# Optimization experiments

Hardware: AMD Instinct MI355X
Metric: run time of the kernel (lower is better)

Reference implementation:

```python
import jax, jax.numpy as jnp
import numpy as np


def _hadamard(n: int) -> np.ndarray:
    # Sylvester construction; n must be a power of 2 (asserted in the torch source).
    H = np.array([[1.0]], dtype=np.float32)
    while H.shape[0] < n:
        H = np.block([[H, H], [H, -H]])
    return (H * (n ** -0.5)).astype(np.float32)


def _rotate_activation(x):
    # hadamard_transform(x, scale=D**-0.5) over the last dim; bf16 in/out like the CUDA kernel.
    D = x.shape[-1]
    H = jnp.asarray(_hadamard(D))
    return (x.astype(jnp.float32) @ H).astype(x.dtype)


def _cu_seqlen_kv_bounds(seq_lens, num_ctx_tokens):
    # Vectorized equivalent of compute_cu_seqlen_kv_bounds_nocache (repeat_interleave -> searchsorted).
    offsets = jnp.concatenate([jnp.zeros(1, jnp.int32), jnp.cumsum(seq_lens).astype(jnp.int32)])
    pos = jnp.arange(num_ctx_tokens, dtype=jnp.int32)
    batch_ids = jnp.searchsorted(offsets, pos, side='right').astype(jnp.int32) - 1
    ks = offsets[batch_ids]                 # start of this token's sequence in packed KV
    ke = ks + (pos - ks) + 1                # causal: local_position + 1 past the start
    return ks, ke


def setup_inputs() -> dict:
    key = jax.random.key(0)
    k1, k2, k3 = jax.random.split(key, 3)
    T, H, D = 2048, 16, 128
    q = jax.random.normal(k1, (T, H, D), dtype=jnp.bfloat16)
    k = jax.random.normal(k2, (T, D), dtype=jnp.bfloat16)
    weights = jax.random.uniform(k3, (T, H), dtype=jnp.float32) * (H ** -0.5)
    seq_lens = jnp.array([1024, 1024], dtype=jnp.int32)
    return {"q": q, "k": k, "weights": weights, "seq_lens": seq_lens, "index_topk": 256}


def reference(q, k, weights, seq_lens, index_topk):
    T = q.shape[0]
    # Hadamard-rotate q and k (lightning indexer activation rotation).
    qr = _rotate_activation(q).astype(jnp.float32)   # [T, H, D]
    kr = _rotate_activation(k).astype(jnp.float32)   # [T, D]
    # Index score: I[t, s] = sum_h w[t, h] * relu(q[t, h] . k[s])
    logits = jnp.einsum('thd,sd->ths', qr, kr)       # [T, H, T]
    scores = jnp.einsum('ths,th->ts', jax.nn.relu(logits), weights)  # [T, T]
    # Causal ragged-batch KV window per token.
    ks, ke = _cu_seqlen_kv_bounds(seq_lens, T)
    pos = jnp.arange(T, dtype=jnp.int32)
    valid = (pos[None, :] >= ks[:, None]) & (pos[None, :] < ke[:, None])
    NEG = jnp.float32(-1e30)
    masked = jnp.where(valid, scores, NEG)
    topk_vals, topk_idx = jax.lax.top_k(masked, index_topk)  # [T, topk]
    return topk_vals, topk_idx
```

## Files before the change

kernel.cpp:

```cpp
#include <hip/hip_runtime.h>
#include <hip/hip_bf16.h>
#include <stdint.h>

typedef __attribute__((ext_vector_type(8))) short short8;
typedef __attribute__((ext_vector_type(4))) float float4_t;

#define DDIM 128
#define SORTN 256
#define LROW 136
#define SCAP 1088
#define NCHT 17

__device__ inline unsigned short f32_to_bf16_rne(float f) {
    uint32_t u = __float_as_uint(f);
    return (unsigned short)((u + 0x7FFFu + ((u >> 16) & 1u)) >> 16);
}
__device__ inline float bf16_to_f32(unsigned short h) {
    return __uint_as_float(((uint32_t)h) << 16);
}
__device__ inline int ks_of(const int* seq_lens, int n_seq, int t) {
    int off = 0, r = 0;
    for (int i = 0; i < n_seq; ++i) {
        int nx = off + seq_lens[i];
        if (t < nx) { r = off; break; }
        off = nx;
    }
    return r;
}

__device__ inline int wave_reduce_add_dpp(int x) {
    x += __builtin_amdgcn_update_dpp(0, x, 0x111, 0xF, 0xF, true);
    x += __builtin_amdgcn_update_dpp(0, x, 0x112, 0xF, 0xF, true);
    x += __builtin_amdgcn_update_dpp(0, x, 0x114, 0xF, 0xF, true);
    x += __builtin_amdgcn_update_dpp(0, x, 0x118, 0xF, 0xF, true);
    x += __builtin_amdgcn_update_dpp(0, x, 0x142, 0xA, 0xF, true);
    x += __builtin_amdgcn_update_dpp(0, x, 0x143, 0xC, 0xF, true);
    return __builtin_amdgcn_readlane(x, 63);
}

__global__ __launch_bounds__(256) void rotate_k_kernel(
        const unsigned short* __restrict__ k, unsigned short* __restrict__ kr, int T) {
    int row = blockIdx.x * 16 + (threadIdx.x >> 4);
    if (row >= T) return;
    int l16 = threadIdx.x & 15;
    short8 in = *(const short8*)(k + (size_t)row * DDIM + 8 * l16);
    float f[8];
    #pragma unroll
    for (int j = 0; j < 8; ++j) f[j] = bf16_to_f32((unsigned short)in[j]);
    #pragma unroll
    for (int b = 1; b <= 4; b <<= 1)
        #pragma unroll
        for (int j = 0; j < 8; ++j)
            if (!(j & b)) { float a = f[j], c = f[j | b]; f[j] = a + c; f[j | b] = a - c; }
    #pragma unroll
    for (int m = 1; m <= 8; m <<= 1) {
        bool hi = (l16 & m) != 0;
        #pragma unroll
        for (int j = 0; j < 8; ++j) {
            float o = __shfl_xor(f[j], m, 64);
            f[j] = hi ? (o - f[j]) : (f[j] + o);
        }
    }
    const float sc = 0.08838834764831845f;
    short8 out;
    #pragma unroll
    for (int j = 0; j < 8; ++j) out[j] = (short)f32_to_bf16_rne(f[j] * sc);
    *(short8*)(kr + (size_t)row * DDIM + 8 * l16) = out;
}

__global__ __launch_bounds__(512, 4) void fused_kernel(
        const unsigned short* __restrict__ q,
        const unsigned short* __restrict__ kr,
        const float* __restrict__ w,
        const int* __restrict__ seq_lens, int n_seq,
        float* __restrict__ out_vals, float* __restrict__ out_idx,
        int T, int H, int K, int Tt) {
    __shared__ __align__(16) unsigned short bL[128 * LROW];
    __shared__ __align__(16) float scw[4][SCAP];

    const int tid  = threadIdx.x;
    const int wv   = tid >> 6, lane = tid & 63;
    const int tok  = wv & 3, half = wv >> 2;
    const int col  = lane & 15, kgrp = lane >> 4;
    const int srow = tid >> 4, sseg = tid & 15;

    const int m     = blockIdx.x;
    const int ttile = (m & 1) ? (Tt - 1 - (m >> 1)) : (m >> 1);
    const int tt0   = ttile * 4;
    const int t_w   = tt0 + tok;
    const bool wvalid = (t_w < T);
    const int t_c  = wvalid ? t_w : T - 1;
    const int ks_w = ks_of(seq_lens, n_seq, t_c);
    const int ke_w = t_c + 1;
    const int n    = ke_w - ks_w;

    const int bks   = ks_of(seq_lens, n_seq, tt0);
    const int bke   = (tt0 + 4 < T) ? (tt0 + 4) : T;
    const int ntile = (bke - bks + 127) >> 7;

    short8 pre[4];
    {
        int kv0 = bks;
        #pragma unroll
        for (int it = 0; it < 4; ++it) {
            int gs = kv0 + srow + 32 * it; if (gs > T - 1) gs = T - 1;
            pre[it] = *(const short8*)(kr + (size_t)gs * DDIM + sseg * 8);
        }
    }

    float f[4][8];
    const unsigned short* qrow = q + ((size_t)t_c * H + col) * DDIM + kgrp * 8;
    #pragma unroll
    for (int kk = 0; kk < 4; ++kk) {
        short8 v = *(const short8*)(qrow + kk * 32);
        #pragma unroll
        for (int j = 0; j < 8; ++j) f[kk][j] = bf16_to_f32((unsigned short)v[j]);
    }
    #pragma unroll
    for (int b = 1; b <= 4; b <<= 1)
        #pragma unroll
        for (int kk = 0; kk < 4; ++kk)
            #pragma unroll
            for (int j = 0; j < 8; ++j)
                if (!(j & b)) { float a = f[kk][j], c = f[kk][j | b];
                                f[kk][j] = a + c; f[kk][j | b] = a - c; }
    #pragma unroll
    for (int kk = 0; kk < 4; ++kk)
        #pragma unroll
        for (int j = 0; j < 8; ++j) {
            float o = __shfl_xor(f[kk][j], 16, 64);
            f[kk][j] = (kgrp & 1) ? (o - f[kk][j]) : (f[kk][j] + o);
        }
    #pragma unroll
    for (int kk = 0; kk < 4; ++kk)
        #pragma unroll
        for (int j = 0; j < 8; ++j) {
            float o = __shfl_xor(f[kk][j], 32, 64);
            f[kk][j] = (kgrp & 2) ? (o - f[kk][j]) : (f[kk][j] + o);
        }
    #pragma unroll
    for (int j = 0; j < 8; ++j) {
        { float a = f[0][j], c = f[1][j]; f[0][j] = a + c; f[1][j] = a - c; }
        { float a = f[2][j], c = f[3][j]; f[2][j] = a + c; f[3][j] = a - c; }
        { float a = f[0][j], c = f[2][j]; f[0][j] = a + c; f[2][j] = a - c; }
        { float a = f[1][j], c = f[3][j]; f[1][j] = a + c; f[3][j] = a - c; }
    }
    short8 afrag[4];
    const float scl = 0.08838834764831845f;
    #pragma unroll
    for (int kk = 0; kk < 4; ++kk)
        #pragma unroll
        for (int j = 0; j < 8; ++j)
            afrag[kk][j] = (short)f32_to_bf16_rne(f[kk][j] * scl);

    float w4[4];
    #pragma unroll
    for (int r = 0; r < 4; ++r) w4[r] = w[(size_t)t_c * H + kgrp * 4 + r];

    #pragma unroll
    for (int it = 0; it < 4; ++it)
        *(short8*)&bL[(srow + 32 * it) * LROW + sseg * 8] = pre[it];
    __syncthreads();

    for (int c = 0; c < ntile; ++c) {
        const int kv0 = bks + c * 128;
        if (c + 1 < ntile) {
            int kvn = kv0 + 128;
            #pragma unroll
            for (int it = 0; it < 4; ++it) {
                int gs = kvn + srow + 32 * it; if (gs > T - 1) gs = T - 1;
                pre[it] = *(const short8*)(kr + (size_t)gs * DDIM + sseg * 8);
            }
        }
        #pragma unroll
        for (int nth = 0; nth < 4; ++nth) {
            const int nt = half * 4 + nth;
            float4_t acc = {0.f, 0.f, 0.f, 0.f};
            #pragma unroll
            for (int kk = 0; kk < 4; ++kk) {
                short8 bf = *(const short8*)&bL[(nt * 16 + col) * LROW + kgrp * 8 + kk * 32];
                acc = __builtin_amdgcn_mfma_f32_16x16x32_bf16(afrag[kk], bf, acc, 0, 0, 0);
            }
            float p = 0.f;
            #pragma unroll
            for (int r = 0; r < 4; ++r) {
                float v = acc[r];
                v = v > 0.f ? v : 0.f;
                p += w4[r] * v;
            }
            p += __shfl_xor(p, 16, 64);
            p += __shfl_xor(p, 32, 64);
            int s = kv0 + nt * 16 + col;
            if (wvalid && lane < 16 && s >= ks_w && s <= t_w)
                scw[tok][s - ks_w] = p;
        }
        __syncthreads();
        if (c + 1 < ntile) {
            #pragma unroll
            for (int it = 0; it < 4; ++it)
                *(short8*)&bL[(srow + 32 * it) * LROW + sseg * 8] = pre[it];
            __syncthreads();
        }
    }

    if (half == 1 || !wvalid) return;

    const int nch = (n + 63) >> 6;
    uint32_t ukey[NCHT];
    #pragma unroll
    for (int c = 0; c < NCHT; ++c) {
        if (c < nch) {
            int i = c * 64 + lane;
            ukey[c] = (i < n) ? __float_as_uint(scw[tok][i]) : 0u;
        } else ukey[c] = 0u;
    }
    unsigned long long* candw = (unsigned long long*)&scw[tok][0];

    const int Keff = (n < K) ? n : K;
    uint32_t ustar = 0;
    int ttake = K;
    if (n > K) {
        uint32_t lo = 0, hi = 0x80000000u;
        for (int it = 0; it < 31; ++it) {
            uint32_t mid = (lo + hi) >> 1;
            int lc = 0;
            #pragma unroll
            for (int c = 0; c < NCHT; ++c)
                if (c < nch) lc += (ukey[c] >= mid) ? 1 : 0;
            int total = wave_reduce_add_dpp(lc);
            if (total >= K) lo = mid; else hi = mid;
        }
        ustar = lo;
        int lg = 0;
        #pragma unroll
        for (int c = 0; c < NCHT; ++c)
            if (c < nch) lg += (ukey[c] > ustar) ? 1 : 0;
        ttake = K - wave_reduce_add_dpp(lg);
    }

    {
        const unsigned long long ltm = (1ull << lane) - 1ull;
        int base = 0, tieBase = 0;
        const bool selAll = (n <= K);
        #pragma unroll
        for (int c = 0; c < NCHT; ++c) {
            if (c < nch) {
                int i = c * 64 + lane;
                bool inb = (i < n);
                uint32_t u = ukey[c];
                bool isGt  = inb && (selAll || u > ustar);
                bool isTie = inb && !selAll && (u == ustar);
                unsigned long long mt = __ballot(isTie);
                int tr = tieBase + (int)__popcll(mt & ltm);
                bool take = isGt || (isTie && tr < ttake);
                unsigned long long mk = __ballot(take);
                if (take) {
                    int pos = base + (int)__popcll(mk & ltm);
                    int s = ks_w + i;
                    if (pos < SORTN)
                        candw[pos] = ((((unsigned long long)u << 11) |
                                       (unsigned long long)(T - 1 - s)) + 1ull);
                }
                base    += (int)__popcll(mk);
                tieBase += (int)__popcll(mt);
            }
        }
        for (int i = Keff + lane; i < SORTN; i += 64) candw[i] = 0ull;
    }

    unsigned long long kreg[4];
    #pragma unroll
    for (int r = 0; r < 4; ++r) kreg[r] = candw[4 * lane + r];

    #define CX(a, b, dsc) { unsigned long long _mx = (a) > (b) ? (a) : (b); \
                            unsigned long long _mn = (a) > (b) ? (b) : (a); \
                            (a) = (dsc) ? _mx : _mn; (b) = (dsc) ? _mn : _mx; }
    #pragma unroll
    for (int size = 2; size <= SORTN; size <<= 1) {
        #pragma unroll
        for (int stride = SORTN >> 1; stride >= 4; stride >>= 1) {
            if (stride > (size >> 1)) continue;
            int lmask = stride >> 2;
            #pragma unroll
            for (int r = 0; r < 4; ++r) {
                int e = 4 * lane + r;
                unsigned long long other = __shfl_xor(kreg[r], lmask, 64);
                bool desc = ((e & size) == 0);
                bool iAmLow = ((e & stride) == 0);
                bool keepMax = (iAmLow == desc);
                kreg[r] = keepMax ? (kreg[r] > other ? kreg[r] : other)
                                  : (kreg[r] < other ? kreg[r] : other);
            }
        }
        if (size >= 4) {
            bool d = (((4 * lane) & size) == 0);
            CX(kreg[0], kreg[2], d);
            CX(kreg[1], kreg[3], d);
            CX(kreg[0], kreg[1], d);
            CX(kreg[2], kreg[3], d);
        } else {
            CX(kreg[0], kreg[1], true);
            CX(kreg[2], kreg[3], false);
        }
    }
    #undef CX

    if (4 * lane < K) {
        float4_t v4, i4;
        #pragma unroll
        for (int r = 0; r < 4; ++r) {
            int e = 4 * lane + r;
            unsigned long long key = kreg[r];
            float v; int idx;
            if (key != 0ull) {
                unsigned long long km1 = key - 1ull;
                v = __uint_as_float((uint32_t)(km1 >> 11));
                idx = T - 1 - (int)(km1 & 0x7FFull);
            } else {
                int pidx = e - Keff;
                idx = (pidx < ks_w) ? pidx : (ke_w + (pidx - ks_w));
                v = -1e30f;
            }
            v4[r] = v; i4[r] = (float)idx;
        }
        *(float4_t*)(out_vals + (size_t)t_w * K + 4 * lane) = v4;
        *(float4_t*)(out_idx  + (size_t)t_w * K + 4 * lane) = i4;
    }
}

extern "C" void kernel_launch(void* const* d_in, const int* in_sizes, int n_in,
                              void* d_out, int out_size, void* d_ws, size_t ws_size,
                              hipStream_t stream) {
    const unsigned short* q = (const unsigned short*)d_in[0];
    const unsigned short* k = (const unsigned short*)d_in[1];
    const float* w          = (const float*)d_in[2];
    const int* seq_lens     = (const int*)d_in[3];
    const int n_seq = in_sizes[3];
    const int T = in_sizes[1] / DDIM;
    const int H = in_sizes[2] / T;
    const int K = out_size / (2 * T);

    unsigned short* kr = (unsigned short*)d_ws;
    float* out_vals = (float*)d_out;
    float* out_idx  = out_vals + (size_t)T * K;

    rotate_k_kernel<<<dim3((T + 15) / 16), dim3(256), 0, stream>>>(k, kr, T);
    const int Tt = (T + 3) / 4;
    fused_kernel<<<dim3(Tt), dim3(512), 0, stream>>>(
        q, kr, w, seq_lens, n_seq, out_vals, out_idx, T, H, K, Tt);
}
```

Measured before the change: 105.4 us.

## Remap MFMA so each wave covers all four tokens and heads per KV strip

Restructures the score GEMM so the MFMA M dimension packs 4 tokens x 4 heads per 16-row fragment. Each wave now holds the rotated Q fragments for all 16 heads of the 4 tokens and handles one 16-column KV strip, reusing each B fragment loaded from LDS across four MFMAs instead of one. The head-weighted ReLU reduction becomes in-lane, which removes the cross-lane shuffles. The cost is four Hadamard rotations per wave instead of one, plus more registers for the Q fragments and weights. SCAP padding is also changed, likely to shift LDS bank mapping.

```diff
diff --git a/kernel.cpp b/kernel.cpp
--- a/kernel.cpp
+++ b/kernel.cpp
@@ -8,7 +8,7 @@
 #define DDIM 128
 #define SORTN 256
 #define LROW 136
-#define SCAP 1088
+#define SCAP 1096
 #define NCHT 17
 
 __device__ inline unsigned short f32_to_bf16_rne(float f) {
@@ -80,82 +80,87 @@
 
     const int tid  = threadIdx.x;
     const int wv   = tid >> 6, lane = tid & 63;
-    const int tok  = wv & 3, half = wv >> 2;
     const int col  = lane & 15, kgrp = lane >> 4;
     const int srow = tid >> 4, sseg = tid & 15;
 
     const int m     = blockIdx.x;
     const int ttile = (m & 1) ? (Tt - 1 - (m >> 1)) : (m >> 1);
     const int tt0   = ttile * 4;
-    const int t_w   = tt0 + tok;
-    const bool wvalid = (t_w < T);
-    const int t_c  = wvalid ? t_w : T - 1;
-    const int ks_w = ks_of(seq_lens, n_seq, t_c);
-    const int ke_w = t_c + 1;
-    const int n    = ke_w - ks_w;
+
+    int t_l = tt0 + kgrp; if (t_l > T - 1) t_l = T - 1;
+    const int ks_l = ks_of(seq_lens, n_seq, t_l);
 
     const int bks   = ks_of(seq_lens, n_seq, tt0);
     const int bke   = (tt0 + 4 < T) ? (tt0 + 4) : T;
     const int ntile = (bke - bks + 127) >> 7;
 
     short8 pre[4];
+    #pragma unroll
+    for (int it = 0; it < 4; ++it) {
+        int gs = bks + srow + 32 * it; if (gs > T - 1) gs = T - 1;
+        pre[it] = *(const short8*)(kr + (size_t)gs * DDIM + sseg * 8);
+    }
+
+    short8 afragA[4][4];
+    const float scl = 0.08838834764831845f;
+    #pragma unroll
+    for (int hb = 0; hb < 4; ++hb) {
+        int tq = tt0 + (col >> 2); if (tq > T - 1) tq = T - 1;
+        int hq = hb * 4 + (col & 3);
+        const unsigned short* qrow = q + ((size_t)tq * H + hq) * DDIM + kgrp * 8;
+        float f[4][8];
+        #pragma unroll
+        for (int kk = 0; kk < 4; ++kk) {
+            short8 v = *(const short8*)(qrow + kk * 32);
+            #pragma unroll
+            for (int j = 0; j < 8; ++j) f[kk][j] = bf16_to_f32((unsigned short)v[j]);
+        }
+        #pragma unroll
+        for (int b = 1; b <= 4; b <<= 1)
+            #pragma unroll
+            for (int kk = 0; kk < 4; ++kk)
+                #pragma unroll
+                for (int j = 0; j < 8; ++j)
+                    if (!(j & b)) { float a = f[kk][j], c = f[kk][j | b];
+                                    f[kk][j] = a + c; f[kk][j | b] = a - c; }
+        #pragma unroll
+        for (int kk = 0; kk < 4; ++kk)
+            #pragma unroll
+            for (int j = 0; j < 8; ++j) {
+                float o = __shfl_xor(f[kk][j], 16, 64);
+                f[kk][j] = (kgrp & 1) ? (o - f[kk][j]) : (f[kk][j] + o);
+            }
+        #pragma unroll
+        for (int kk = 0; kk < 4; ++kk)
+            #pragma unroll
+            for (int j = 0; j < 8; ++j) {
+                float o = __shfl_xor(f[kk][j], 32, 64);
+                f[kk][j] = (kgrp & 2) ? (o - f[kk][j]) : (f[kk][j] + o);
+            }
+        #pragma unroll
+        for (int j = 0; j < 8; ++j) {
+            { float a = f[0][j], c = f[1][j]; f[0][j] = a + c; f[1][j] = a - c; }
+            { float a = f[2][j], c = f[3][j]; f[2][j] = a + c; f[3][j] = a - c; }
+            { float a = f[0][j], c = f[2][j]; f[0][j] = a + c; f[2][j] = a - c; }
+            { float a = f[1][j], c = f[3][j]; f[1][j] = a + c; f[3][j] = a - c; }
+        }
+        #pragma unroll
+        for (int kk = 0; kk < 4; ++kk)
+            #pragma unroll
+            for (int j = 0; j < 8; ++j)
+                afragA[hb][kk][j] = (short)f32_to_bf16_rne(f[kk][j] * scl);
+    }
+
+    float w16[16];
     {
-        int kv0 = bks;
-        #pragma unroll
-        for (int it = 0; it < 4; ++it) {
-            int gs = kv0 + srow + 32 * it; if (gs > T - 1) gs = T - 1;
-            pre[it] = *(const short8*)(kr + (size_t)gs * DDIM + sseg * 8);
-        }
-    }
-
-    float f[4][8];
-    const unsigned short* qrow = q + ((size_t)t_c * H + col) * DDIM + kgrp * 8;
-    #pragma unroll
-    for (int kk = 0; kk < 4; ++kk) {
-        short8 v = *(const short8*)(qrow + kk * 32);
-        #pragma unroll
-        for (int j = 0; j < 8; ++j) f[kk][j] = bf16_to_f32((unsigned short)v[j]);
-    }
-    #pragma unroll
-    for (int b = 1; b <= 4; b <<= 1)
-        #pragma unroll
-        for (int kk = 0; kk < 4; ++kk)
-            #pragma unroll
-            for (int j = 0; j < 8; ++j)
-                if (!(j & b)) { float a = f[kk][j], c = f[kk][j | b];
-                                f[kk][j] = a + c; f[kk][j | b] = a - c; }
-    #pragma unroll
-    for (int kk = 0; kk < 4; ++kk)
-        #pragma unroll
-        for (int j = 0; j < 8; ++j) {
-            float o = __shfl_xor(f[kk][j], 16, 64);
-            f[kk][j] = (kgrp & 1) ? (o - f[kk][j]) : (f[kk][j] + o);
-        }
-    #pragma unroll
-    for (int kk = 0; kk < 4; ++kk)
-        #pragma unroll
-        for (int j = 0; j < 8; ++j) {
-            float o = __shfl_xor(f[kk][j], 32, 64);
-            f[kk][j] = (kgrp & 2) ? (o - f[kk][j]) : (f[kk][j] + o);
-        }
-    #pragma unroll
-    for (int j = 0; j < 8; ++j) {
-        { float a = f[0][j], c = f[1][j]; f[0][j] = a + c; f[1][j] = a - c; }
-        { float a = f[2][j], c = f[3][j]; f[2][j] = a + c; f[3][j] = a - c; }
-        { float a = f[0][j], c = f[2][j]; f[0][j] = a + c; f[2][j] = a - c; }
-        { float a = f[1][j], c = f[3][j]; f[1][j] = a + c; f[3][j] = a - c; }
-    }
-    short8 afrag[4];
-    const float scl = 0.08838834764831845f;
-    #pragma unroll
-    for (int kk = 0; kk < 4; ++kk)
-        #pragma unroll
-        for (int j = 0; j < 8; ++j)
-            afrag[kk][j] = (short)f32_to_bf16_rne(f[kk][j] * scl);
-
-    float w4[4];
-    #pragma unroll
-    for (int r = 0; r < 4; ++r) w4[r] = w[(size_t)t_c * H + kgrp * 4 + r];
+        const float4* wp = (const float4*)(w + (size_t)t_l * H);
+        #pragma unroll
+        for (int i = 0; i < 4; ++i) {
+            float4 v = wp[i];
+            w16[4 * i] = v.x; w16[4 * i + 1] = v.y;
+            w16[4 * i + 2] = v.z; w16[4 * i + 3] = v.w;
+        }
+    }
 
     #pragma unroll
     for (int it = 0; it < 4; ++it)
@@ -172,27 +177,28 @@
                 pre[it] = *(const short8*)(kr + (size_t)gs * DDIM + sseg * 8);
             }
         }
-        #pragma unroll
-        for (int nth = 0; nth < 4; ++nth) {
-            const int nt = half * 4 + nth;
-            float4_t acc = {0.f, 0.f, 0.f, 0.f};
+        {
+            float4_t a0 = {0.f,0.f,0.f,0.f}, a1 = a0, a2 = a0, a3 = a0;
             #pragma unroll
             for (int kk = 0; kk < 4; ++kk) {
-                short8 bf = *(const short8*)&bL[(nt * 16 + col) * LROW + kgrp * 8 + kk * 32];
-                acc = __builtin_amdgcn_mfma_f32_16x16x32_bf16(afrag[kk], bf, acc, 0, 0, 0);
+                short8 bf = *(const short8*)&bL[(wv * 16 + col) * LROW + kgrp * 8 + kk * 32];
+                a0 = __builtin_amdgcn_mfma_f32_16x16x32_bf16(afragA[0][kk], bf, a0, 0, 0, 0);
+                a1 = __builtin_amdgcn_mfma_f32_16x16x32_bf16(afragA[1][kk], bf, a1, 0, 0, 0);
+                a2 = __builtin_amdgcn_mfma_f32_16x16x32_bf16(afragA[2][kk], bf, a2, 0, 0, 0);
+                a3 = __builtin_amdgcn_mfma_f32_16x16x32_bf16(afragA[3][kk], bf, a3, 0, 0, 0);
             }
             float p = 0.f;
             #pragma unroll
             for (int r = 0; r < 4; ++r) {
-                float v = acc[r];
-                v = v > 0.f ? v : 0.f;
-                p += w4[r] * v;
-            }
-            p += __shfl_xor(p, 16, 64);
-            p += __shfl_xor(p, 32, 64);
-            int s = kv0 + nt * 16 + col;
-            if (wvalid && lane < 16 && s >= ks_w && s <= t_w)
-                scw[tok][s - ks_w] = p;
+                float v0 = a0[r] > 0.f ? a0[r] : 0.f;
+                float v1 = a1[r] > 0.f ? a1[r] : 0.f;
+                float v2 = a2[r] > 0.f ? a2[r] : 0.f;
+                float v3 = a3[r] > 0.f ? a3[r] : 0.f;
+                p += w16[r] * v0 + w16[4 + r] * v1 + w16[8 + r] * v2 + w16[12 + r] * v3;
+            }
+            int s = kv0 + wv * 16 + col;
+            if (s >= ks_l && s <= t_l && (tt0 + kgrp) < T)
+                scw[kgrp][s - ks_l] = p;
         }
         __syncthreads();
         if (c + 1 < ntile) {
@@ -203,7 +209,12 @@
         }
     }
 
-    if (half == 1 || !wvalid) return;
+    if (wv >= 4) return;
+    const int t_w = tt0 + wv;
+    if (t_w >= T) return;
+    const int ks_w = ks_of(seq_lens, n_seq, t_w);
+    const int ke_w = t_w + 1;
+    const int n    = ke_w - ks_w;
 
     const int nch = (n + 63) >> 6;
     uint32_t ukey[NCHT];
@@ -211,10 +222,10 @@
     for (int c = 0; c < NCHT; ++c) {
         if (c < nch) {
             int i = c * 64 + lane;
-            ukey[c] = (i < n) ? __float_as_uint(scw[tok][i]) : 0u;
+            ukey[c] = (i < n) ? __float_as_uint(scw[wv][i]) : 0u;
         } else ukey[c] = 0u;
     }
-    unsigned long long* candw = (unsigned long long*)&scw[tok][0];
+    unsigned long long* candw = (unsigned long long*)&scw[wv][0];
 
     const int Keff = (n < K) ? n : K;
     uint32_t ustar = 0;
```

Result: slower. 196.1 us (+86.0%).
